# Performance work log

Hardware: AMD Instinct MI355X
Metric: run time of the kernel (lower is better)

The kernel has to match this reference:

```python
import jax, jax.numpy as jnp
import numpy as np

R = 8      # num_dilation_rates
B = 32
C_IN = 21
C = 128    # C_out
L = 4096
K = 2      # kernel_size


def _causal_conv(x, w, dilation, pad, length):
    # x: [B, C, L], w: [Co, Ci, K]. Left-pad by `pad`, dilated valid conv, keep first L.
    # Matches Causal_conv1d: type 'A' -> pad=K(=2); type 'B' -> pad=dilation*(K-1)+1.
    y = jax.lax.conv_general_dilated(
        x, w, window_strides=(1,), padding=[(pad, 0)],
        rhs_dilation=(dilation,), dimension_numbers=('NCH', 'OIH', 'NCH'))
    return y[:, :, :length]


def setup_inputs() -> dict:
    key = jax.random.key(0)
    ks = jax.random.split(key, 10)
    s = 0.1  # small init scale (stands in for xavier)
    return {
        'x': jax.random.normal(ks[0], (B, C_IN, L), jnp.float32),
        'z': jax.random.normal(ks[1], (B, 1, L), jnp.float32),
        'w0': jax.random.normal(ks[2], (C, C_IN), jnp.float32) * s,          # causal_blocks[0] 1x1 conv
        'b0': jnp.zeros((C,), jnp.float32),
        'signal_w': jax.random.normal(ks[3], (R, C, C, K), jnp.float32) * s,  # dilated kernel-2 convs
        'gate_w': jax.random.normal(ks[4], (R, C, C, K), jnp.float32) * s,
        'cond_signal_w': jax.random.normal(ks[5], (R, C), jnp.float32) * s,   # Conv1d(1, C, 1) weights
        'cond_gate_w': jax.random.normal(ks[6], (R, C), jnp.float32) * s,
        'res_w': jax.random.normal(ks[7], (R, C, C), jnp.float32) * s,        # 1x1 residual convs
        'skip_w': jax.random.normal(ks[8], (R, C, C), jnp.float32) * s,       # 1x1 skip convs
    }


def reference(x, z, w0, b0, signal_w, gate_w, cond_signal_w, cond_gate_w, res_w, skip_w):
    length = x.shape[2]
    # initial 1x1 conv with bias
    h = jnp.einsum('oi,bil->bol', w0, x) + b0[None, :, None]
    orig = h
    cum_skip = jnp.zeros_like(h)
    zf = z[:, 0, :]  # [B, L]
    n_rates = signal_w.shape[0]
    for ii in range(n_rates):
        d = 2 ** ii
        pad = K if ii == 0 else d * (K - 1) + 1  # mask 'A' for layer 0, 'B' otherwise
        signal = _causal_conv(h, signal_w[ii], d, pad, length) \
            + jnp.einsum('o,bl->bol', cond_signal_w[ii], zf)
        gate = _causal_conv(h, gate_w[ii], d, pad, length) \
            + jnp.einsum('o,bl->bol', cond_gate_w[ii], zf)
        g = signal * jax.nn.sigmoid(gate)                      # gated activation
        skip = jnp.einsum('oi,bil->bol', skip_w[ii], g)
        res = jnp.einsum('oi,bil->bol', res_w[ii], g)
        h = (orig + res) if ii == 0 else (res + g)             # matches torch control flow
        cum_skip = cum_skip + skip
    return h, cum_skip
```

## Files before the change

kernel.cpp:

```cpp
#include <hip/hip_runtime.h>
#include <hip/hip_bf16.h>

#define RR 8
#define BB 32
#define CIN 21
#define CC 128
#define LL 4096
#define TT 64
#define GP 136
#define PADT 132
#define LP (LL + PADT)

typedef short s16x8 __attribute__((ext_vector_type(8)));
typedef float f32x4 __attribute__((ext_vector_type(4)));
typedef unsigned int __attribute__((address_space(1))) gu32;
typedef unsigned int __attribute__((address_space(3))) lu32;

__device__ __forceinline__ unsigned short f2b(float f) {
    __hip_bfloat16 h = __float2bfloat16(f);
    return *reinterpret_cast<unsigned short*>(&h);
}
__device__ __forceinline__ float b2f(unsigned short u) {
    __hip_bfloat16 h;
    *reinterpret_cast<unsigned short*>(&h) = u;
    return __bfloat162float(h);
}
__device__ __forceinline__ unsigned int packsplit(float v) {
    unsigned short hi = f2b(v);
    unsigned short lo = f2b(v - b2f(hi));
    return ((unsigned int)hi << 16) | (unsigned int)lo;
}
__device__ __forceinline__ float unpacksum(unsigned int u) {
    return b2f((unsigned short)(u >> 16)) + b2f((unsigned short)(u & 0xffffu));
}

__device__ __forceinline__ void unpack2(uint4 u0, uint4 u1, s16x8& hi, s16x8& lo) {
    union { int i[4]; s16x8 v; } H, L;
    H.i[0] = __builtin_amdgcn_perm(u0.y, u0.x, 0x07060302u);
    L.i[0] = __builtin_amdgcn_perm(u0.y, u0.x, 0x05040100u);
    H.i[1] = __builtin_amdgcn_perm(u0.w, u0.z, 0x07060302u);
    L.i[1] = __builtin_amdgcn_perm(u0.w, u0.z, 0x05040100u);
    H.i[2] = __builtin_amdgcn_perm(u1.y, u1.x, 0x07060302u);
    L.i[2] = __builtin_amdgcn_perm(u1.y, u1.x, 0x05040100u);
    H.i[3] = __builtin_amdgcn_perm(u1.w, u1.z, 0x07060302u);
    L.i[3] = __builtin_amdgcn_perm(u1.w, u1.z, 0x05040100u);
    hi = H.v; lo = L.v;
}

__global__ void prep_kernel(const float* __restrict__ sw, const float* __restrict__ gw,
                            const float* __restrict__ skw, const float* __restrict__ rew,
                            unsigned short* __restrict__ WsgH, unsigned short* __restrict__ WsgL,
                            unsigned short* __restrict__ WkrH, unsigned short* __restrict__ WkrL) {
    int idx = blockIdx.x * 256 + threadIdx.x;
    int r = idx >> 16;
    int rem = idx & 65535;
    int o = rem >> 8;
    int k = rem & 255;
    int c = k & 127;
    int tap = k >> 7;
    float v = (o < 128) ? sw[(((r * 128 + o) * 128 + c) << 1) + tap]
                        : gw[(((r * 128 + (o - 128)) * 128 + c) << 1) + tap];
    unsigned short hi = f2b(v);
    WsgH[idx] = hi;
    WsgL[idx] = f2b(v - b2f(hi));
    if (idx < RR * 256 * 128) {
        int r2 = idx >> 15;
        int rem2 = idx & 32767;
        int o2 = rem2 >> 7;
        int c2 = rem2 & 127;
        float v2 = (o2 < 128) ? skw[(r2 * 128 + o2) * 128 + c2]
                              : rew[(r2 * 128 + (o2 - 128)) * 128 + c2];
        unsigned short hi2 = f2b(v2);
        WkrH[idx] = hi2;
        WkrL[idx] = f2b(v2 - b2f(hi2));
    }
}

__global__ void zero_pad_kernel(unsigned int* __restrict__ hA, unsigned int* __restrict__ hB) {
    int idx = blockIdx.x * 256 + threadIdx.x;
    int c = idx & 127;
    int r = (idx >> 7) % PADT;
    int b = idx / (PADT * 128);
    size_t off = ((size_t)b * LP + r) * CC + c;
    hA[off] = 0u;
    hB[off] = 0u;
}

__global__ void proj_kernel(const float* __restrict__ x, const float* __restrict__ w0,
                            const float* __restrict__ b0, unsigned int* __restrict__ h0) {
    int idx = blockIdx.x * 256 + threadIdx.x;
    int c = idx & 127;
    int t = (idx >> 7) & (LL - 1);
    int b = idx >> 19;
    const float* xb = x + (size_t)b * CIN * LL + t;
    const float* w = w0 + c * CIN;
    float acc = b0[c];
#pragma unroll
    for (int i = 0; i < CIN; i++) acc = fmaf(w[i], xb[i * LL], acc);
    h0[((size_t)b * LP + PADT + t) * CC + c] = packsplit(acc);
}

__global__ void __launch_bounds__(512, 4) layer_kernel(
    const unsigned int* __restrict__ hcur,
    unsigned int* __restrict__ hnext,
    float* __restrict__ skipbuf,
    const unsigned short* __restrict__ WsgH, const unsigned short* __restrict__ WsgL,
    const unsigned short* __restrict__ WkrH, const unsigned short* __restrict__ WkrL,
    const float* __restrict__ csw, const float* __restrict__ cgw,
    const float* __restrict__ z,
    float* __restrict__ out,
    int off0, int first, int last) {
    __shared__ unsigned int sBuf[16384];
    unsigned short* sGhi = (unsigned short*)sBuf;
    unsigned short* sGlo = sGhi + TT * GP;

    int tid = threadIdx.x;
    int b = blockIdx.x >> 6;
    int t0 = (blockIdx.x & 63) * TT;

    int wave = tid >> 6;
    int lane = tid & 63;
    int l15 = lane & 15;
    int quad = lane >> 4;

    const unsigned int* hb = hcur + (size_t)b * LP * CC;

    {
        const unsigned int* src0 = hb + (size_t)(PADT + t0 - off0) * CC;
        const unsigned int* src1 = hb + (size_t)(PADT + t0 - 1) * CC;
#pragma unroll
        for (int jj = 0; jj < 8; jj++) {
            int flat = tid + 512 * jj;
            int row = (flat >> 5) & 63;
            int ud = flat & 31;
            const unsigned int* srcw = (jj < 4) ? src0 : src1;
            const unsigned int* gp = srcw + (size_t)row * CC + ((ud ^ (row & 7)) << 2);
            unsigned int* lp = sBuf + flat * 4;
            __builtin_amdgcn_global_load_lds((const gu32*)gp, (lu32*)lp, 16, 0, 0);
        }
    }
    __syncthreads();

    f32x4 acc1[4][2];
#pragma unroll
    for (int m = 0; m < 4; m++)
#pragma unroll
        for (int n = 0; n < 2; n++) acc1[m][n] = (f32x4){0.f, 0.f, 0.f, 0.f};

#pragma unroll
    for (int kk = 0; kk < 8; kk++) {
        const int win = kk >> 2;
        const int U = (kk & 3) * 8 + quad * 2;
        s16x8 Ah[4], Al[4];
#pragma unroll
        for (int m = 0; m < 4; m++) {
            int r = m * 16 + l15;
            const unsigned int* base = sBuf + win * 8192 + r * 128;
            int s = r & 7;
            uint4 x0 = *(const uint4*)(base + ((U ^ s) << 2));
            uint4 x1 = *(const uint4*)(base + (((U + 1) ^ s) << 2));
            unpack2(x0, x1, Ah[m], Al[m]);
        }
#pragma unroll
        for (int n = 0; n < 2; n++) {
            int o = (wave + 8 * n) * 16 + l15;
            s16x8 Bh = *(const s16x8*)(WsgH + o * 256 + kk * 32 + quad * 8);
            s16x8 Bl = *(const s16x8*)(WsgL + o * 256 + kk * 32 + quad * 8);
#pragma unroll
            for (int m = 0; m < 4; m++) {
                acc1[m][n] = __builtin_amdgcn_mfma_f32_16x16x32_bf16(Ah[m], Bh, acc1[m][n], 0, 0, 0);
                acc1[m][n] = __builtin_amdgcn_mfma_f32_16x16x32_bf16(Al[m], Bh, acc1[m][n], 0, 0, 0);
                acc1[m][n] = __builtin_amdgcn_mfma_f32_16x16x32_bf16(Ah[m], Bl, acc1[m][n], 0, 0, 0);
            }
        }
    }

    float g[4][4];
    {
        const float* zb = z + (size_t)b * LL + t0;
        float cs = csw[wave * 16 + l15];
        float cg = cgw[wave * 16 + l15];
#pragma unroll
        for (int m = 0; m < 4; m++)
#pragma unroll
            for (int reg = 0; reg < 4; reg++) {
                float zv = zb[m * 16 + quad * 4 + reg];
                float s = fmaf(cs, zv, acc1[m][0][reg]);
                float t = fmaf(cg, zv, acc1[m][1][reg]);
                g[m][reg] = s / (1.f + __expf(-t));
            }
    }
    __syncthreads();

    {
        int c = wave * 16 + l15;
#pragma unroll
        for (int m = 0; m < 4; m++)
#pragma unroll
            for (int reg = 0; reg < 4; reg++) {
                int tl = m * 16 + quad * 4 + reg;
                float gv = g[m][reg];
                unsigned short hi = f2b(gv);
                sGhi[tl * GP + c] = hi;
                sGlo[tl * GP + c] = f2b(gv - b2f(hi));
            }
    }
    __syncthreads();

    f32x4 acc2[4][2];
#pragma unroll
    for (int m = 0; m < 4; m++)
#pragma unroll
        for (int n = 0; n < 2; n++) acc2[m][n] = (f32x4){0.f, 0.f, 0.f, 0.f};

#pragma unroll
    for (int kk = 0; kk < 4; kk++) {
        s16x8 Ah[4], Al[4];
#pragma unroll
        for (int m = 0; m < 4; m++) {
            int off = (m * 16 + l15) * GP + kk * 32 + quad * 8;
            Ah[m] = *(const s16x8*)(sGhi + off);
            Al[m] = *(const s16x8*)(sGlo + off);
        }
#pragma unroll
        for (int n = 0; n < 2; n++) {
            int o2 = (wave + 8 * n) * 16 + l15;
            s16x8 Bh = *(const s16x8*)(WkrH + o2 * 128 + kk * 32 + quad * 8);
            s16x8 Bl = *(const s16x8*)(WkrL + o2 * 128 + kk * 32 + quad * 8);
#pragma unroll
            for (int m = 0; m < 4; m++) {
                acc2[m][n] = __builtin_amdgcn_mfma_f32_16x16x32_bf16(Ah[m], Bh, acc2[m][n], 0, 0, 0);
                acc2[m][n] = __builtin_amdgcn_mfma_f32_16x16x32_bf16(Al[m], Bh, acc2[m][n], 0, 0, 0);
                acc2[m][n] = __builtin_amdgcn_mfma_f32_16x16x32_bf16(Ah[m], Bl, acc2[m][n], 0, 0, 0);
            }
        }
    }

#pragma unroll
    for (int m = 0; m < 4; m++) {
        int c = wave * 16 + l15;
#pragma unroll
        for (int reg = 0; reg < 4; reg++) {
            int t = t0 + m * 16 + quad * 4 + reg;
            size_t hidx = ((size_t)b * LP + PADT + t) * CC + c;
            size_t sidx = ((size_t)b * LL + t) * CC + c;
            float skp = acc2[m][0][reg];
            float res = acc2[m][1][reg];
            float hv, sv;
            if (first) {
                hv = res + unpacksum(hcur[hidx]);
                sv = skp;
            } else {
                hv = res + g[m][reg];
                sv = skp + skipbuf[sidx];
            }
            if (last) {
                size_t oidx = ((size_t)b * CC + c) * LL + t;
                out[oidx] = hv;
                out[(size_t)BB * CC * LL + oidx] = sv;
            } else {
                hnext[hidx] = packsplit(hv);
                skipbuf[sidx] = sv;
            }
        }
    }
}

extern "C" void kernel_launch(void* const* d_in, const int* in_sizes, int n_in,
                              void* d_out, int out_size, void* d_ws, size_t ws_size,
                              hipStream_t stream) {
    const float* x = (const float*)d_in[0];
    const float* z = (const float*)d_in[1];
    const float* w0 = (const float*)d_in[2];
    const float* b0 = (const float*)d_in[3];
    const float* sw = (const float*)d_in[4];
    const float* gw = (const float*)d_in[5];
    const float* csw = (const float*)d_in[6];
    const float* cgw = (const float*)d_in[7];
    const float* rew = (const float*)d_in[8];
    const float* skw = (const float*)d_in[9];

    const size_t HSZ = (size_t)BB * LP * CC;
    const size_t NCL = (size_t)BB * CC * LL;
    unsigned int* hA = (unsigned int*)d_ws;
    unsigned int* hB = hA + HSZ;
    float* skipb = (float*)(hB + HSZ);
    unsigned short* WsgH = (unsigned short*)(skipb + NCL);
    unsigned short* WsgL = WsgH + (size_t)RR * 256 * 256;
    unsigned short* WkrH = WsgL + (size_t)RR * 256 * 256;
    unsigned short* WkrL = WkrH + (size_t)RR * 256 * 128;

    prep_kernel<<<RR * 256 * 256 / 256, 256, 0, stream>>>(sw, gw, skw, rew, WsgH, WsgL, WkrH, WkrL);
    zero_pad_kernel<<<BB * PADT * 128 / 256, 256, 0, stream>>>(hA, hB);
    proj_kernel<<<NCL / 256, 256, 0, stream>>>(x, w0, b0, hA);

    unsigned int* hc = hA;
    unsigned int* hn = hB;
    for (int ii = 0; ii < RR; ii++) {
        int d = 1 << ii;
        int off0 = d + 1;
        layer_kernel<<<BB * (LL / TT), 512, 0, stream>>>(
            hc, hn, skipb,
            WsgH + (size_t)ii * 256 * 256, WsgL + (size_t)ii * 256 * 256,
            WkrH + (size_t)ii * 256 * 128, WkrL + (size_t)ii * 256 * 128,
            csw + ii * CC, cgw + ii * CC, z,
            (float*)d_out, off0, ii == 0 ? 1 : 0, ii == RR - 1 ? 1 : 0);
        unsigned int* tmp = hc; hc = hn; hn = tmp;
    }
}
```

Before: 1.322 ms.

## Make layer kernel persistent over tiles with double-buffered async LDS prefetch

Each block now handles 8 consecutive 64-step time tiles instead of one. It double-buffers the shared-memory h window so the async global-to-LDS load for the next tile runs during the current tile's epilogue. Skip and residual-source loads are hoisted ahead of the prefetch. The grid shrinks eightfold, LDS per block doubles and launch bounds occupancy drops from 4 to 2, trading occupancy and parallelism for overlap of load latency with compute.

New measurement: 1.570 ms. +18.7%, slower.

```diff
diff --git a/kernel.cpp b/kernel.cpp
--- a/kernel.cpp
+++ b/kernel.cpp
@@ -7,6 +7,7 @@
 #define CC 128
 #define LL 4096
 #define TT 64
+#define NTILE 8
 #define GP 136
 #define PADT 132
 #define LP (LL + PADT)
@@ -100,7 +101,7 @@
     h0[((size_t)b * LP + PADT + t) * CC + c] = packsplit(acc);
 }
 
-__global__ void __launch_bounds__(512, 4) layer_kernel(
+__global__ void __launch_bounds__(512, 2) layer_kernel(
     const unsigned int* __restrict__ hcur,
     unsigned int* __restrict__ hnext,
     float* __restrict__ skipbuf,
@@ -110,13 +111,11 @@
     const float* __restrict__ z,
     float* __restrict__ out,
     int off0, int first, int last) {
-    __shared__ unsigned int sBuf[16384];
-    unsigned short* sGhi = (unsigned short*)sBuf;
-    unsigned short* sGlo = sGhi + TT * GP;
+    __shared__ unsigned int sBuf[32768];
 
     int tid = threadIdx.x;
-    int b = blockIdx.x >> 6;
-    int t0 = (blockIdx.x & 63) * TT;
+    int b = blockIdx.x >> 3;
+    int chunk = blockIdx.x & 7;
 
     int wave = tid >> 6;
     int lane = tid & 63;
@@ -125,12 +124,15 @@
 
     const unsigned int* hb = hcur + (size_t)b * LP * CC;
 
+    const int sflat0 = tid;
+
     {
+        int t0 = chunk * (NTILE * TT);
         const unsigned int* src0 = hb + (size_t)(PADT + t0 - off0) * CC;
         const unsigned int* src1 = hb + (size_t)(PADT + t0 - 1) * CC;
 #pragma unroll
         for (int jj = 0; jj < 8; jj++) {
-            int flat = tid + 512 * jj;
+            int flat = sflat0 + 512 * jj;
             int row = (flat >> 5) & 63;
             int ud = flat & 31;
             const unsigned int* srcw = (jj < 4) ? src0 : src1;
@@ -139,128 +141,177 @@
             __builtin_amdgcn_global_load_lds((const gu32*)gp, (lu32*)lp, 16, 0, 0);
         }
     }
-    __syncthreads();
-
-    f32x4 acc1[4][2];
-#pragma unroll
-    for (int m = 0; m < 4; m++)
-#pragma unroll
-        for (int n = 0; n < 2; n++) acc1[m][n] = (f32x4){0.f, 0.f, 0.f, 0.f};
-
-#pragma unroll
-    for (int kk = 0; kk < 8; kk++) {
-        const int win = kk >> 2;
-        const int U = (kk & 3) * 8 + quad * 2;
-        s16x8 Ah[4], Al[4];
+
+    for (int it = 0; it < NTILE; it++) {
+        const int cur = it & 1;
+        const int t0 = chunk * (NTILE * TT) + it * TT;
+        unsigned int* W = sBuf + cur * 16384;
+        unsigned short* sGhi = (unsigned short*)W;
+        unsigned short* sGlo = sGhi + TT * GP;
+
+        asm volatile("s_waitcnt vmcnt(0)" ::: "memory");
+        __builtin_amdgcn_s_barrier();
+        __builtin_amdgcn_sched_barrier(0);
+
+        f32x4 acc1[4][2];
+#pragma unroll
+        for (int m = 0; m < 4; m++)
+#pragma unroll
+            for (int n = 0; n < 2; n++) acc1[m][n] = (f32x4){0.f, 0.f, 0.f, 0.f};
+
+#pragma unroll
+        for (int kk = 0; kk < 8; kk++) {
+            const int win = kk >> 2;
+            const int U = (kk & 3) * 8 + quad * 2;
+            s16x8 Ah[4], Al[4];
+#pragma unroll
+            for (int m = 0; m < 4; m++) {
+                int r = m * 16 + l15;
+                const unsigned int* base = W + win * 8192 + r * 128;
+                int s = r & 7;
+                uint4 x0 = *(const uint4*)(base + ((U ^ s) << 2));
+                uint4 x1 = *(const uint4*)(base + (((U + 1) ^ s) << 2));
+                unpack2(x0, x1, Ah[m], Al[m]);
+            }
+#pragma unroll
+            for (int n = 0; n < 2; n++) {
+                int o = (wave + 8 * n) * 16 + l15;
+                s16x8 Bh = *(const s16x8*)(WsgH + o * 256 + kk * 32 + quad * 8);
+                s16x8 Bl = *(const s16x8*)(WsgL + o * 256 + kk * 32 + quad * 8);
+#pragma unroll
+                for (int m = 0; m < 4; m++) {
+                    acc1[m][n] = __builtin_amdgcn_mfma_f32_16x16x32_bf16(Ah[m], Bh, acc1[m][n], 0, 0, 0);
+                    acc1[m][n] = __builtin_amdgcn_mfma_f32_16x16x32_bf16(Al[m], Bh, acc1[m][n], 0, 0, 0);
+                    acc1[m][n] = __builtin_amdgcn_mfma_f32_16x16x32_bf16(Ah[m], Bl, acc1[m][n], 0, 0, 0);
+                }
+            }
+        }
+
+        float g[4][4];
+        {
+            const float* zb = z + (size_t)b * LL + t0;
+            float cs = csw[wave * 16 + l15];
+            float cg = cgw[wave * 16 + l15];
+#pragma unroll
+            for (int m = 0; m < 4; m++)
+#pragma unroll
+                for (int reg = 0; reg < 4; reg++) {
+                    float zv = zb[m * 16 + quad * 4 + reg];
+                    float s = fmaf(cs, zv, acc1[m][0][reg]);
+                    float t = fmaf(cg, zv, acc1[m][1][reg]);
+                    g[m][reg] = s / (1.f + __expf(-t));
+                }
+        }
+
+        __builtin_amdgcn_s_barrier();
+        __builtin_amdgcn_sched_barrier(0);
+        {
+            int c = wave * 16 + l15;
+#pragma unroll
+            for (int m = 0; m < 4; m++)
+#pragma unroll
+                for (int reg = 0; reg < 4; reg++) {
+                    int tl = m * 16 + quad * 4 + reg;
+                    float gv = g[m][reg];
+                    unsigned short hi = f2b(gv);
+                    sGhi[tl * GP + c] = hi;
+                    sGlo[tl * GP + c] = f2b(gv - b2f(hi));
+                }
+        }
+        asm volatile("s_waitcnt lgkmcnt(0)" ::: "memory");
+        __builtin_amdgcn_s_barrier();
+        __builtin_amdgcn_sched_barrier(0);
+
+        f32x4 acc2[4][2];
+#pragma unroll
+        for (int m = 0; m < 4; m++)
+#pragma unroll
+            for (int n = 0; n < 2; n++) acc2[m][n] = (f32x4){0.f, 0.f, 0.f, 0.f};
+
+#pragma unroll
+        for (int kk = 0; kk < 4; kk++) {
+            s16x8 Ah[4], Al[4];
+#pragma unroll
+            for (int m = 0; m < 4; m++) {
+                int off = (m * 16 + l15) * GP + kk * 32 + quad * 8;
+                Ah[m] = *(const s16x8*)(sGhi + off);
+                Al[m] = *(const s16x8*)(sGlo + off);
+            }
+#pragma unroll
+            for (int n = 0; n < 2; n++) {
+                int o2 = (wave + 8 * n) * 16 + l15;
+                s16x8 Bh = *(const s16x8*)(WkrH + o2 * 128 + kk * 32 + quad * 8);
+                s16x8 Bl = *(const s16x8*)(WkrL + o2 * 128 + kk * 32 + quad * 8);
+#pragma unroll
+                for (int m = 0; m < 4; m++) {
+                    acc2[m][n] = __builtin_amdgcn_mfma_f32_16x16x32_bf16(Ah[m], Bh, acc2[m][n], 0, 0, 0);
+                    acc2[m][n] = __builtin_amdgcn_mfma_f32_16x16x32_bf16(Al[m], Bh, acc2[m][n], 0, 0, 0);
+                    acc2[m][n] = __builtin_amdgcn_mfma_f32_16x16x32_bf16(Ah[m], Bl, acc2[m][n], 0, 0, 0);
+                }
+            }
+        }
+
+        float sk[4][4];
+        {
+            int c = wave * 16 + l15;
+            if (first) {
+#pragma unroll
+                for (int m = 0; m < 4; m++)
+#pragma unroll
+                    for (int reg = 0; reg < 4; reg++) {
+                        int t = t0 + m * 16 + quad * 4 + reg;
+                        sk[m][reg] = unpacksum(hcur[((size_t)b * LP + PADT + t) * CC + c]);
+                    }
+            } else {
+#pragma unroll
+                for (int m = 0; m < 4; m++)
+#pragma unroll
+                    for (int reg = 0; reg < 4; reg++) {
+                        int t = t0 + m * 16 + quad * 4 + reg;
+                        sk[m][reg] = skipbuf[((size_t)b * LL + t) * CC + c];
+                    }
+            }
+        }
+        __builtin_amdgcn_sched_barrier(0);
+
+        if (it + 1 < NTILE) {
+            int t1 = t0 + TT;
+            unsigned int* Wn = sBuf + (cur ^ 1) * 16384;
+            const unsigned int* src0 = hb + (size_t)(PADT + t1 - off0) * CC;
+            const unsigned int* src1 = hb + (size_t)(PADT + t1 - 1) * CC;
+#pragma unroll
+            for (int jj = 0; jj < 8; jj++) {
+                int flat = sflat0 + 512 * jj;
+                int row = (flat >> 5) & 63;
+                int ud = flat & 31;
+                const unsigned int* srcw = (jj < 4) ? src0 : src1;
+                const unsigned int* gp = srcw + (size_t)row * CC + ((ud ^ (row & 7)) << 2);
+                unsigned int* lp = Wn + flat * 4;
+                __builtin_amdgcn_global_load_lds((const gu32*)gp, (lu32*)lp, 16, 0, 0);
+            }
+        }
+        __builtin_amdgcn_sched_barrier(0);
+
 #pragma unroll
         for (int m = 0; m < 4; m++) {
-            int r = m * 16 + l15;
-            const unsigned int* base = sBuf + win * 8192 + r * 128;
-            int s = r & 7;
-            uint4 x0 = *(const uint4*)(base + ((U ^ s) << 2));
-            uint4 x1 = *(const uint4*)(base + (((U + 1) ^ s) << 2));
-            unpack2(x0, x1, Ah[m], Al[m]);
-        }
-#pragma unroll
-        for (int n = 0; n < 2; n++) {
-            int o = (wave + 8 * n) * 16 + l15;
-            s16x8 Bh = *(const s16x8*)(WsgH + o * 256 + kk * 32 + quad * 8);
-            s16x8 Bl = *(const s16x8*)(WsgL + o * 256 + kk * 32 + quad * 8);
-#pragma unroll
-            for (int m = 0; m < 4; m++) {
-                acc1[m][n] = __builtin_amdgcn_mfma_f32_16x16x32_bf16(Ah[m], Bh, acc1[m][n], 0, 0, 0);
-                acc1[m][n] = __builtin_amdgcn_mfma_f32_16x16x32_bf16(Al[m], Bh, acc1[m][n], 0, 0, 0);
-                acc1[m][n] = __builtin_amdgcn_mfma_f32_16x16x32_bf16(Ah[m], Bl, acc1[m][n], 0, 0, 0);
-            }
-        }
-    }
-
-    float g[4][4];
-    {
-        const float* zb = z + (size_t)b * LL + t0;
-        float cs = csw[wave * 16 + l15];
-        float cg = cgw[wave * 16 + l15];
-#pragma unroll
-        for (int m = 0; m < 4; m++)
+            int c = wave * 16 + l15;
 #pragma unroll
             for (int reg = 0; reg < 4; reg++) {
-                float zv = zb[m * 16 + quad * 4 + reg];
-                float s = fmaf(cs, zv, acc1[m][0][reg]);
-                float t = fmaf(cg, zv, acc1[m][1][reg]);
-                g[m][reg] = s / (1.f + __expf(-t));
-            }
-    }
-    __syncthreads();
-
-    {
-        int c = wave * 16 + l15;
-#pragma unroll
-        for (int m = 0; m < 4; m++)
-#pragma unroll
-            for (int reg = 0; reg < 4; reg++) {
-                int tl = m * 16 + quad * 4 + reg;
-                float gv = g[m][reg];
-                unsigned short hi = f2b(gv);
-                sGhi[tl * GP + c] = hi;
-                sGlo[tl * GP + c] = f2b(gv - b2f(hi));
-            }
-    }
-    __syncthreads();
-
-    f32x4 acc2[4][2];
-#pragma unroll
-    for (int m = 0; m < 4; m++)
-#pragma unroll
-        for (int n = 0; n < 2; n++) acc2[m][n] = (f32x4){0.f, 0.f, 0.f, 0.f};
-
-#pragma unroll
-    for (int kk = 0; kk < 4; kk++) {
-        s16x8 Ah[4], Al[4];
-#pragma unroll
-        for (int m = 0; m < 4; m++) {
-            int off = (m * 16 + l15) * GP + kk * 32 + quad * 8;
-            Ah[m] = *(const s16x8*)(sGhi + off);
-            Al[m] = *(const s16x8*)(sGlo + off);
-        }
-#pragma unroll
-        for (int n = 0; n < 2; n++) {
-            int o2 = (wave + 8 * n) * 16 + l15;
-            s16x8 Bh = *(const s16x8*)(WkrH + o2 * 128 + kk * 32 + quad * 8);
-            s16x8 Bl = *(const s16x8*)(WkrL + o2 * 128 + kk * 32 + quad * 8);
-#pragma unroll
-            for (int m = 0; m < 4; m++) {
-                acc2[m][n] = __builtin_amdgcn_mfma_f32_16x16x32_bf16(Ah[m], Bh, acc2[m][n], 0, 0, 0);
-                acc2[m][n] = __builtin_amdgcn_mfma_f32_16x16x32_bf16(Al[m], Bh, acc2[m][n], 0, 0, 0);
-                acc2[m][n] = __builtin_amdgcn_mfma_f32_16x16x32_bf16(Ah[m], Bl, acc2[m][n], 0, 0, 0);
-            }
-        }
-    }
-
-#pragma unroll
-    for (int m = 0; m < 4; m++) {
-        int c = wave * 16 + l15;
-#pragma unroll
-        for (int reg = 0; reg < 4; reg++) {
-            int t = t0 + m * 16 + quad * 4 + reg;
-            size_t hidx = ((size_t)b * LP + PADT + t) * CC + c;
-            size_t sidx = ((size_t)b * LL + t) * CC + c;
-            float skp = acc2[m][0][reg];
-            float res = acc2[m][1][reg];
-            float hv, sv;
-            if (first) {
-                hv = res + unpacksum(hcur[hidx]);
-                sv = skp;
-            } else {
-                hv = res + g[m][reg];
-                sv = skp + skipbuf[sidx];
-            }
-            if (last) {
-                size_t oidx = ((size_t)b * CC + c) * LL + t;
-                out[oidx] = hv;
-                out[(size_t)BB * CC * LL + oidx] = sv;
-            } else {
-                hnext[hidx] = packsplit(hv);
-                skipbuf[sidx] = sv;
+                int t = t0 + m * 16 + quad * 4 + reg;
+                size_t hidx = ((size_t)b * LP + PADT + t) * CC + c;
+                float skp = acc2[m][0][reg];
+                float res = acc2[m][1][reg];
+                float hv, sv;
+                if (first) { hv = res + sk[m][reg]; sv = skp; }
+                else       { hv = res + g[m][reg];  sv = skp + sk[m][reg]; }
+                if (last) {
+                    size_t oidx = ((size_t)b * CC + c) * LL + t;
+                    out[oidx] = hv;
+                    out[(size_t)BB * CC * LL + oidx] = sv;
+                } else {
+                    hnext[hidx] = packsplit(hv);
+                    skipbuf[((size_t)b * LL + t) * CC + c] = sv;
+                }
             }
         }
     }
@@ -299,7 +350,7 @@
     for (int ii = 0; ii < RR; ii++) {
         int d = 1 << ii;
         int off0 = d + 1;
-        layer_kernel<<<BB * (LL / TT), 512, 0, stream>>>(
+        layer_kernel<<<BB * (LL / TT / NTILE), 512, 0, stream>>>(
             hc, hn, skipb,
             WsgH + (size_t)ii * 256 * 256, WsgL + (size_t)ii * 256 * 256,
             WkrH + (size_t)ii * 256 * 128, WkrL + (size_t)ii * 256 * 128,
```

## Prefetch skip/residual values early and split conv loads to overlap with MFMA

Applied to the files above, without the earlier changes.

Moves the per-element loads of the skip buffer (or the original h for the first layer) to the start of the kernel so their latency is hidden behind the GEMM work. The two dilated-conv tap windows are now loaded in separate batches, with a partial vmcnt wait so the first tap's MFMAs start while the second tap's global-to-LDS loads are still in flight. Full __syncthreads are replaced with raw s_barrier plus explicit waitcnts. This costs 16 extra live registers per thread and relies on hand-placed waitcnt counts being correct.

New measurement: 1.428 ms. 1.08x slower.

```diff
diff --git a/kernel.cpp b/kernel.cpp
--- a/kernel.cpp
+++ b/kernel.cpp
@@ -124,22 +124,55 @@
     int quad = lane >> 4;
 
     const unsigned int* hb = hcur + (size_t)b * LP * CC;
+    const int cch = wave * 16 + l15;
+
+    unsigned int skraw[4][4];
+    if (first) {
+#pragma unroll
+        for (int m = 0; m < 4; m++)
+#pragma unroll
+            for (int reg = 0; reg < 4; reg++) {
+                int t = t0 + m * 16 + quad * 4 + reg;
+                skraw[m][reg] = hb[(size_t)(PADT + t) * CC + cch];
+            }
+    } else {
+        const unsigned int* sbb = (const unsigned int*)skipbuf + (size_t)b * LL * CC;
+#pragma unroll
+        for (int m = 0; m < 4; m++)
+#pragma unroll
+            for (int reg = 0; reg < 4; reg++) {
+                int t = t0 + m * 16 + quad * 4 + reg;
+                skraw[m][reg] = sbb[(size_t)t * CC + cch];
+            }
+    }
+    __builtin_amdgcn_sched_barrier(0);
 
     {
         const unsigned int* src0 = hb + (size_t)(PADT + t0 - off0) * CC;
+#pragma unroll
+        for (int jj = 0; jj < 4; jj++) {
+            int flat = tid + 512 * jj;
+            int row = flat >> 5;
+            int ud = flat & 31;
+            const unsigned int* gp = src0 + (size_t)row * CC + ((ud ^ (row & 7)) << 2);
+            __builtin_amdgcn_global_load_lds((const gu32*)gp, (lu32*)(sBuf + flat * 4), 16, 0, 0);
+        }
+        __builtin_amdgcn_sched_barrier(0);
         const unsigned int* src1 = hb + (size_t)(PADT + t0 - 1) * CC;
 #pragma unroll
-        for (int jj = 0; jj < 8; jj++) {
+        for (int jj = 0; jj < 4; jj++) {
             int flat = tid + 512 * jj;
-            int row = (flat >> 5) & 63;
+            int row = flat >> 5;
             int ud = flat & 31;
-            const unsigned int* srcw = (jj < 4) ? src0 : src1;
-            const unsigned int* gp = srcw + (size_t)row * CC + ((ud ^ (row & 7)) << 2);
-            unsigned int* lp = sBuf + flat * 4;
-            __builtin_amdgcn_global_load_lds((const gu32*)gp, (lu32*)lp, 16, 0, 0);
-        }
-    }
-    __syncthreads();
+            const unsigned int* gp = src1 + (size_t)row * CC + ((ud ^ (row & 7)) << 2);
+            __builtin_amdgcn_global_load_lds((const gu32*)gp, (lu32*)(sBuf + 8192 + flat * 4), 16, 0, 0);
+        }
+    }
+    __builtin_amdgcn_sched_barrier(0);
+
+    asm volatile("s_waitcnt vmcnt(4)" ::: "memory");
+    __builtin_amdgcn_s_barrier();
+    __builtin_amdgcn_sched_barrier(0);
 
     f32x4 acc1[4][2];
 #pragma unroll
@@ -148,14 +181,13 @@
         for (int n = 0; n < 2; n++) acc1[m][n] = (f32x4){0.f, 0.f, 0.f, 0.f};
 
 #pragma unroll
-    for (int kk = 0; kk < 8; kk++) {
-        const int win = kk >> 2;
-        const int U = (kk & 3) * 8 + quad * 2;
+    for (int kk = 0; kk < 4; kk++) {
+        const int U = kk * 8 + quad * 2;
         s16x8 Ah[4], Al[4];
 #pragma unroll
         for (int m = 0; m < 4; m++) {
             int r = m * 16 + l15;
-            const unsigned int* base = sBuf + win * 8192 + r * 128;
+            const unsigned int* base = sBuf + r * 128;
             int s = r & 7;
             uint4 x0 = *(const uint4*)(base + ((U ^ s) << 2));
             uint4 x1 = *(const uint4*)(base + (((U + 1) ^ s) << 2));
@@ -175,11 +207,42 @@
         }
     }
 
+    asm volatile("s_waitcnt vmcnt(0)" ::: "memory");
+    __builtin_amdgcn_s_barrier();
+    __builtin_amdgcn_sched_barrier(0);
+
+#pragma unroll
+    for (int kk = 4; kk < 8; kk++) {
+        const int U = (kk & 3) * 8 + quad * 2;
+        s16x8 Ah[4], Al[4];
+#pragma unroll
+        for (int m = 0; m < 4; m++) {
+            int r = m * 16 + l15;
+            const unsigned int* base = sBuf + 8192 + r * 128;
+            int s = r & 7;
+            uint4 x0 = *(const uint4*)(base + ((U ^ s) << 2));
+            uint4 x1 = *(const uint4*)(base + (((U + 1) ^ s) << 2));
+            unpack2(x0, x1, Ah[m], Al[m]);
+        }
+#pragma unroll
+        for (int n = 0; n < 2; n++) {
+            int o = (wave + 8 * n) * 16 + l15;
+            s16x8 Bh = *(const s16x8*)(WsgH + o * 256 + kk * 32 + quad * 8);
+            s16x8 Bl = *(const s16x8*)(WsgL + o * 256 + kk * 32 + quad * 8);
+#pragma unroll
+            for (int m = 0; m < 4; m++) {
+                acc1[m][n] = __builtin_amdgcn_mfma_f32_16x16x32_bf16(Ah[m], Bh, acc1[m][n], 0, 0, 0);
+                acc1[m][n] = __builtin_amdgcn_mfma_f32_16x16x32_bf16(Al[m], Bh, acc1[m][n], 0, 0, 0);
+                acc1[m][n] = __builtin_amdgcn_mfma_f32_16x16x32_bf16(Ah[m], Bl, acc1[m][n], 0, 0, 0);
+            }
+        }
+    }
+
     float g[4][4];
     {
         const float* zb = z + (size_t)b * LL + t0;
-        float cs = csw[wave * 16 + l15];
-        float cg = cgw[wave * 16 + l15];
+        float cs = csw[cch];
+        float cg = cgw[cch];
 #pragma unroll
         for (int m = 0; m < 4; m++)
 #pragma unroll
@@ -190,10 +253,10 @@
                 g[m][reg] = s / (1.f + __expf(-t));
             }
     }
-    __syncthreads();
+    __builtin_amdgcn_s_barrier();
+    __builtin_amdgcn_sched_barrier(0);
 
     {
-        int c = wave * 16 + l15;
 #pragma unroll
         for (int m = 0; m < 4; m++)
 #pragma unroll
@@ -201,11 +264,13 @@
                 int tl = m * 16 + quad * 4 + reg;
                 float gv = g[m][reg];
                 unsigned short hi = f2b(gv);
-                sGhi[tl * GP + c] = hi;
-                sGlo[tl * GP + c] = f2b(gv - b2f(hi));
-            }
-    }
-    __syncthreads();
+                sGhi[tl * GP + cch] = hi;
+                sGlo[tl * GP + cch] = f2b(gv - b2f(hi));
+            }
+    }
+    asm volatile("s_waitcnt lgkmcnt(0)" ::: "memory");
+    __builtin_amdgcn_s_barrier();
+    __builtin_amdgcn_sched_barrier(0);
 
     f32x4 acc2[4][2];
 #pragma unroll
@@ -238,29 +303,27 @@
 
 #pragma unroll
     for (int m = 0; m < 4; m++) {
-        int c = wave * 16 + l15;
 #pragma unroll
         for (int reg = 0; reg < 4; reg++) {
             int t = t0 + m * 16 + quad * 4 + reg;
-            size_t hidx = ((size_t)b * LP + PADT + t) * CC + c;
-            size_t sidx = ((size_t)b * LL + t) * CC + c;
+            size_t hidx = ((size_t)b * LP + PADT + t) * CC + cch;
             float skp = acc2[m][0][reg];
             float res = acc2[m][1][reg];
             float hv, sv;
             if (first) {
-                hv = res + unpacksum(hcur[hidx]);
+                hv = res + unpacksum(skraw[m][reg]);
                 sv = skp;
             } else {
                 hv = res + g[m][reg];
-                sv = skp + skipbuf[sidx];
+                sv = skp + __uint_as_float(skraw[m][reg]);
             }
             if (last) {
-                size_t oidx = ((size_t)b * CC + c) * LL + t;
+                size_t oidx = ((size_t)b * CC + cch) * LL + t;
                 out[oidx] = hv;
                 out[(size_t)BB * CC * LL + oidx] = sv;
             } else {
                 hnext[hidx] = packsplit(hv);
-                skipbuf[sidx] = sv;
+                skipbuf[((size_t)b * LL + t) * CC + cch] = sv;
             }
         }
     }
```
